# Performance work log

Measured on AMD Instinct MI355X. Metric: run time of the kernel, lower is better.

## Reference

```python
import jax, jax.numpy as jnp
import numpy as np
import math

D = 768      # dim_model
H = 12       # num_heads
DK = D // H  # dim_q = dim_k = 64
F = 3072     # dim_feedforward
B, S = 4, 2048
EPS = 1e-5


def layer_norm(x, gamma, beta):
    mu = jnp.mean(x, axis=-1, keepdims=True)
    var = jnp.mean(jnp.square(x - mu), axis=-1, keepdims=True)
    return (x - mu) * jax.lax.rsqrt(var + EPS) * gamma + beta


def setup_inputs() -> dict:
    key = jax.random.key(0)
    ks = jax.random.split(key, 16)
    s = 0.02
    return {
        "source": jax.random.normal(ks[0], (B, S, D), jnp.float32),
        # per-head QKV projections stacked over heads: [H, D, DK]
        "Wq": jax.random.normal(ks[1], (H, D, DK), jnp.float32) * s,
        "bq": jnp.zeros((H, DK), jnp.float32),
        "Wk": jax.random.normal(ks[2], (H, D, DK), jnp.float32) * s,
        "bk": jnp.zeros((H, DK), jnp.float32),
        "Wv": jax.random.normal(ks[3], (H, D, DK), jnp.float32) * s,
        "bv": jnp.zeros((H, DK), jnp.float32),
        "Wo": jax.random.normal(ks[4], (H * DK, D), jnp.float32) * s,
        "bo": jnp.zeros((D,), jnp.float32),
        "g1": jnp.ones((D,), jnp.float32),
        "be1": jnp.zeros((D,), jnp.float32),
        "W1": jax.random.normal(ks[5], (D, F), jnp.float32) * s,
        "bf1": jnp.zeros((F,), jnp.float32),
        "W2": jax.random.normal(ks[6], (F, D), jnp.float32) * s,
        "bf2": jnp.zeros((D,), jnp.float32),
        "g2": jnp.ones((D,), jnp.float32),
        "be2": jnp.zeros((D,), jnp.float32),
    }


def reference(source, Wq, bq, Wk, bk, Wv, bv, Wo, bo, g1, be1, W1, bf1, W2, bf2, g2, be2):
    x = source
    # batched-over-heads QKV (original loops over heads; same math)
    q = jnp.einsum("bsd,hdk->bhsk", x, Wq) + bq[:, None, :]
    k = jnp.einsum("bsd,hdk->bhsk", x, Wk) + bk[:, None, :]
    v = jnp.einsum("bsd,hdk->bhsk", x, Wv) + bv[:, None, :]
    scale = math.sqrt(DK)
    scores = jnp.einsum("bhsk,bhtk->bhst", q, k) / scale  # [B,H,S,S]
    probs = jax.nn.softmax(scores, axis=-1)
    attn = jnp.einsum("bhst,bhtk->bhsk", probs, v)        # [B,H,S,DK]
    # concat heads along feature dim: [B,S,H*DK]
    cat = attn.transpose(0, 2, 1, 3).reshape(B, S, H * DK)
    mha = cat @ Wo + bo
    x1 = layer_norm(x + mha, g1, be1)  # dropout=0 / eval mode
    ffn = jax.nn.relu(x1 @ W1 + bf1) @ W2 + bf2
    return layer_norm(x1 + ffn, g2, be2)
```

## Files before the change

### kernel.cpp

```cpp
#include <hip/hip_runtime.h>
#include <stdint.h>

#define B_ 4
#define S_ 2048
#define D_ 768
#define H_ 12
#define DK_ 64
#define F_ 3072

typedef __bf16 bf16x8 __attribute__((ext_vector_type(8)));
typedef unsigned short u16x8 __attribute__((ext_vector_type(8)));
typedef float f32x4 __attribute__((ext_vector_type(4)));

__device__ inline unsigned short f2bf(float f) {
    union { float f; unsigned u; } v; v.f = f;
    unsigned r = (v.u + 0x7FFFu + ((v.u >> 16) & 1u)) >> 16;
    return (unsigned short)r;
}
__device__ inline float b2f(unsigned short u) {
    union { unsigned u; float f; } v; v.u = ((unsigned)u) << 16;
    return v.f;
}
__device__ inline bf16x8 as_bf(u16x8 v) { return __builtin_bit_cast(bf16x8, v); }
__device__ inline f32x4 mfma16(u16x8 a, u16x8 b, f32x4 c) {
    return __builtin_amdgcn_mfma_f32_16x16x32_bf16(as_bf(a), as_bf(b), c, 0, 0, 0);
}
__device__ inline void gld16(const unsigned short* g, unsigned short* l) {
    __builtin_amdgcn_global_load_lds(
        (__attribute__((address_space(1))) void*)(unsigned short*)g,
        (__attribute__((address_space(3))) void*)l, 16, 0, 0);
}
__device__ inline float fast_exp2(float x) { return __builtin_amdgcn_exp2f(x); }

__global__ __launch_bounds__(256) void prep_k(const float* __restrict__ src,
                                              unsigned short* __restrict__ XBF,
                                              const float* __restrict__ bq,
                                              const float* __restrict__ bk,
                                              const float* __restrict__ bv,
                                              float* __restrict__ BQKV,
                                              const float* __restrict__ Wq,
                                              const float* __restrict__ Wk,
                                              const float* __restrict__ Wv,
                                              const float* __restrict__ Wo,
                                              const float* __restrict__ W1,
                                              const float* __restrict__ W2,
                                              unsigned short* __restrict__ WQT,
                                              unsigned short* __restrict__ WOT,
                                              unsigned short* __restrict__ W1T,
                                              unsigned short* __restrict__ W2T) {
    __shared__ float tile[32][33];
    int bid = blockIdx.x;
    const int t = threadIdx.x;

    if (bid < 6144) {
        int i = (bid * 256 + t) * 4;
        float4 v = *(const float4*)(src + i);
        XBF[i] = f2bf(v.x); XBF[i+1] = f2bf(v.y); XBF[i+2] = f2bf(v.z); XBF[i+3] = f2bf(v.w);
        return;
    }
    bid -= 6144;
    if (bid < 9) {
        int i = bid * 256 + t;
        if (i < 2304) {
            const float* s = (i < 768) ? bq : (i < 1536 ? bk : bv);
            BQKV[i] = s[i % 768];
        }
        return;
    }
    bid -= 9;

    const float* ip; unsigned short* op;
    int inRS, outRS, bx, by;
    if (bid < 1728) {
        int sel = bid / 576; int rem = bid - sel * 576;
        int z = rem / 48; int r2 = rem - z * 48;
        by = r2 >> 1; bx = r2 & 1;
        ip  = (sel == 0 ? Wq : (sel == 1 ? Wk : Wv)) + (long)z * 49152;
        op  = WQT + (long)sel * 589824 + (long)z * 49152;
        inRS = 64; outRS = 768;
    } else {
        bid -= 1728;
        if (bid < 576) {
            by = bid / 24; bx = bid - by * 24;
            ip = Wo; op = WOT; inRS = 768; outRS = 768;
        } else {
            bid -= 576;
            if (bid < 2304) {
                by = bid / 96; bx = bid - by * 96;
                ip = W1; op = W1T; inRS = 3072; outRS = 768;
            } else {
                bid -= 2304;
                by = bid / 24; bx = bid - by * 24;
                ip = W2; op = W2T; inRS = 768; outRS = 3072;
            }
        }
    }
    const int c0 = bx * 32, r0 = by * 32;
    const int tx = t & 31, ty = t >> 5;
    #pragma unroll
    for (int i = 0; i < 32; i += 8)
        tile[ty + i][tx] = ip[(long)(r0 + ty + i) * inRS + c0 + tx];
    __syncthreads();
    #pragma unroll
    for (int i = 0; i < 32; i += 8)
        op[(long)(c0 + ty + i) * outRS + r0 + tx] = f2bf(tile[tx][ty + i]);
}

template<bool OUTBF, bool RELU, bool HASRES, bool SPLIT2>
__global__ __launch_bounds__(256, 3) void gemm_k(const unsigned short* __restrict__ A,
                                                 const unsigned short* __restrict__ Bt,
                                                 const float* __restrict__ bias,
                                                 const float* __restrict__ res,
                                                 void* __restrict__ outp,
                                                 float* __restrict__ outp2,
                                                 int M, int N, int K) {
    __shared__ unsigned short As[8192];
    __shared__ unsigned short Bs[8192];
    const int tid = threadIdx.x;
    const int w = tid >> 6, lane = tid & 63;
    const int m = lane & 15, quad = lane >> 4;
    const int wm = (w >> 1) * 64, wn = (w & 1) * 64;
    const long m0 = (long)blockIdx.x * 128, n0 = (long)blockIdx.y * 128;

    int koff = 0, kend = K;
    bool lead = true;
    if (SPLIT2) {
        const int Kh = K >> 1, z = blockIdx.z;
        koff = z * Kh; kend = koff + Kh; lead = (z == 0);
    }

    const int rowc = tid >> 2, colc = (tid & 3) * 8;
    const unsigned short* aG0 = A + (m0 + rowc) * K + colc;
    const unsigned short* aG1 = A + (m0 + rowc + 64) * K + colc;
    const unsigned short* bG0 = Bt + (n0 + rowc) * K + colc;
    const unsigned short* bG1 = Bt + (n0 + rowc + 64) * K + colc;

    const f32x4 fz = {0.f, 0.f, 0.f, 0.f};
    f32x4 acc[4][4];
    #pragma unroll
    for (int i = 0; i < 4; i++)
        #pragma unroll
        for (int j = 0; j < 4; j++) acc[i][j] = fz;

    for (int k0 = koff; k0 < kend; k0 += 64) {
        __syncthreads();
        #pragma unroll
        for (int ks = 0; ks < 2; ks++) {
            const int kc = k0 + ks * 32;
            gld16(aG0 + kc, As + ks*4096 + w*512);
            gld16(aG1 + kc, As + ks*4096 + 2048 + w*512);
            gld16(bG0 + kc, Bs + ks*4096 + w*512);
            gld16(bG1 + kc, Bs + ks*4096 + 2048 + w*512);
        }
        __syncthreads();
        #pragma unroll
        for (int ks = 0; ks < 2; ks++) {
            u16x8 af[4], bfr[4];
            #pragma unroll
            for (int i = 0; i < 4; i++) af[i] = *(const u16x8*)&As[ks*4096 + (wm + i*16 + m)*32 + quad*8];
            #pragma unroll
            for (int j = 0; j < 4; j++) bfr[j] = *(const u16x8*)&Bs[ks*4096 + (wn + j*16 + m)*32 + quad*8];
            #pragma unroll
            for (int i = 0; i < 4; i++)
                #pragma unroll
                for (int j = 0; j < 4; j++)
                    acc[i][j] = mfma16(af[i], bfr[j], acc[i][j]);
        }
    }

    #pragma unroll
    for (int j = 0; j < 4; j++) {
        const long col = n0 + wn + j*16 + m;
        const float bv = lead ? bias[col] : 0.0f;
        #pragma unroll
        for (int i = 0; i < 4; i++) {
            #pragma unroll
            for (int r = 0; r < 4; r++) {
                const long row = m0 + wm + i*16 + quad*4 + r;
                float v = acc[i][j][r] + bv;
                if (HASRES) { if (lead) v += res[row * N + col]; }
                if (RELU)   v = fmaxf(v, 0.0f);
                if (SPLIT2) {
                    float* o = lead ? (float*)outp : outp2;
                    o[row * N + col] = v;
                } else if (OUTBF) {
                    ((unsigned short*)outp)[row * N + col] = f2bf(v);
                } else {
                    ((float*)outp)[row * N + col] = v;
                }
            }
        }
    }
}

__global__ __launch_bounds__(256, 3) void attn_k(const unsigned short* __restrict__ qkv,
                                                 unsigned short* __restrict__ cat) {
    __shared__ unsigned short Kl[2][4096];
    __shared__ unsigned short Vt[2][64 * 68];
    __shared__ unsigned short Pl[4][32 * 72];

    const int tid = threadIdx.x, w = tid >> 6, lane = tid & 63;
    const int m = lane & 15, quad = lane >> 4;
    const int b = blockIdx.y / H_, h = blockIdx.y % H_;
    const int q0 = blockIdx.x * 128 + w * 32;
    const long rb = (long)b * S_;
    const int LD = 3 * D_;

    const unsigned short* kb = qkv + rb * (long)LD + h * DK_ + D_;
    const unsigned short* vb = qkv + rb * (long)LD + h * DK_ + 2 * D_;

    const int krow = tid >> 2, kcol = (tid & 3) * 8;

    const float QS = 0.125f * 1.4426950408889634f;
    u16x8 qf[2][2];
    #pragma unroll
    for (int s = 0; s < 2; s++)
        #pragma unroll
        for (int ks = 0; ks < 2; ks++) {
            const unsigned short* qp = qkv + (rb + q0 + s*16 + m) * (long)LD + h*DK_ + ks*32 + quad*8;
            u16x8 raw = *(const u16x8*)qp;
            u16x8 sc;
            #pragma unroll
            for (int j = 0; j < 8; j++) sc[j] = f2bf(b2f(raw[j]) * QS);
            qf[s][ks] = sc;
        }

    const int vpr = (tid >> 3) * 2;
    const int vd  = (tid & 7) * 8;

    gld16(kb + (long)krow * LD + kcol,      &Kl[0][w * 512]);
    gld16(kb + (long)krow * LD + 32 + kcol, &Kl[0][2048 + w * 512]);
    {
        u16x8 v0 = *(const u16x8*)(vb + (long)(vpr)     * LD + vd);
        u16x8 v1 = *(const u16x8*)(vb + (long)(vpr + 1) * LD + vd);
        #pragma unroll
        for (int j = 0; j < 8; j++) {
            unsigned pk = (unsigned)v0[j] | ((unsigned)v1[j] << 16);
            *(unsigned*)&Vt[0][(vd + j)*68 + vpr] = pk;
        }
    }

    const f32x4 fz = {0.f, 0.f, 0.f, 0.f};
    float lrow[2] = {0.f, 0.f};
    f32x4 oacc[2][4];
    #pragma unroll
    for (int s = 0; s < 2; s++)
        #pragma unroll
        for (int o = 0; o < 4; o++) oacc[s][o] = fz;

    const int NC = S_ / 64;
    for (int c = 0; c < NC; c++) {
        const int kv0 = c * 64;
        const bool havenext = (c + 1 < NC);
        __syncthreads();

        const unsigned short* kcur = Kl[c & 1];
        const unsigned short* vcur = Vt[c & 1];

        if (havenext) {
            unsigned short* kn_ = Kl[(c + 1) & 1];
            gld16(kb + (long)(kv0 + 64 + krow) * LD + kcol,      kn_ + w * 512);
            gld16(kb + (long)(kv0 + 64 + krow) * LD + 32 + kcol, kn_ + 2048 + w * 512);
        }
        const int kvn = havenext ? kv0 + 64 : kv0;
        u16x8 nv0 = *(const u16x8*)(vb + (long)(kvn + vpr)     * LD + vd);
        u16x8 nv1 = *(const u16x8*)(vb + (long)(kvn + vpr + 1) * LD + vd);

        f32x4 st[2][4];
        #pragma unroll
        for (int s = 0; s < 2; s++)
            #pragma unroll
            for (int t = 0; t < 4; t++) st[s][t] = fz;
        #pragma unroll
        for (int t = 0; t < 4; t++) {
            u16x8 kf0 = *(const u16x8*)&kcur[(t*16 + m)*32 + quad*8];
            u16x8 kf1 = *(const u16x8*)&kcur[2048 + (t*16 + m)*32 + quad*8];
            st[0][t] = mfma16(kf0, qf[0][0], st[0][t]);
            st[0][t] = mfma16(kf1, qf[0][1], st[0][t]);
            st[1][t] = mfma16(kf0, qf[1][0], st[1][t]);
            st[1][t] = mfma16(kf1, qf[1][1], st[1][t]);
        }

        #pragma unroll
        for (int s = 0; s < 2; s++) {
            float su = 0.f;
            #pragma unroll
            for (int t = 0; t < 4; t++) {
                float p0 = fast_exp2(st[s][t][0]);
                float p1 = fast_exp2(st[s][t][1]);
                float p2 = fast_exp2(st[s][t][2]);
                float p3 = fast_exp2(st[s][t][3]);
                su += (p0 + p1) + (p2 + p3);
                unsigned a0 = __builtin_bit_cast(unsigned, p0) + 0x8000u;
                unsigned a1 = __builtin_bit_cast(unsigned, p1) + 0x8000u;
                unsigned a2 = __builtin_bit_cast(unsigned, p2) + 0x8000u;
                unsigned a3 = __builtin_bit_cast(unsigned, p3) + 0x8000u;
                uint2 pk;
                pk.x = __builtin_amdgcn_perm(a1, a0, 0x07060302u);
                pk.y = __builtin_amdgcn_perm(a3, a2, 0x07060302u);
                *(uint2*)&Pl[w][(s*16 + m)*72 + t*16 + quad*4] = pk;
            }
            lrow[s] += su;
        }

        __asm__ volatile("s_waitcnt lgkmcnt(0)" ::: "memory");

        u16x8 pf[2][2];
        #pragma unroll
        for (int s = 0; s < 2; s++)
            #pragma unroll
            for (int ks = 0; ks < 2; ks++)
                pf[s][ks] = *(const u16x8*)&Pl[w][(s*16 + m)*72 + ks*32 + quad*8];

        #pragma unroll
        for (int o = 0; o < 4; o++)
            #pragma unroll
            for (int ks = 0; ks < 2; ks++) {
                union { u16x8 v; uint2 d[2]; } vf;
                vf.d[0] = *(const uint2*)&vcur[(o*16 + m)*68 + ks*32 + quad*8];
                vf.d[1] = *(const uint2*)&vcur[(o*16 + m)*68 + ks*32 + quad*8 + 4];
                oacc[0][o] = mfma16(vf.v, pf[0][ks], oacc[0][o]);
                oacc[1][o] = mfma16(vf.v, pf[1][ks], oacc[1][o]);
            }

        if (havenext) {
            unsigned short* vtn = Vt[(c + 1) & 1];
            #pragma unroll
            for (int j = 0; j < 8; j++) {
                unsigned pk = (unsigned)nv0[j] | ((unsigned)nv1[j] << 16);
                *(unsigned*)&vtn[(vd + j)*68 + vpr] = pk;
            }
        }
    }

    #pragma unroll
    for (int s = 0; s < 2; s++) {
        lrow[s] += __shfl_xor(lrow[s], 16);
        lrow[s] += __shfl_xor(lrow[s], 32);
        const float inv = 1.0f / lrow[s];
        unsigned short* cp = cat + (rb + q0 + s*16 + m) * (long)D_ + h*DK_ + quad*4;
        #pragma unroll
        for (int o = 0; o < 4; o++) {
            unsigned short h0 = f2bf(oacc[s][o][0] * inv);
            unsigned short h1 = f2bf(oacc[s][o][1] * inv);
            unsigned short h2 = f2bf(oacc[s][o][2] * inv);
            unsigned short h3 = f2bf(oacc[s][o][3] * inv);
            uint2 pk;
            pk.x = (unsigned)h0 | ((unsigned)h1 << 16);
            pk.y = (unsigned)h2 | ((unsigned)h3 << 16);
            *(uint2*)(cp + o*16) = pk;
        }
    }
}

__global__ __launch_bounds__(256) void ln_k(const float* __restrict__ in,
                                            const float* __restrict__ in2,
                                            const float* __restrict__ g,
                                            const float* __restrict__ be,
                                            float* __restrict__ outF,
                                            unsigned short* __restrict__ outB) {
    __shared__ float sm[4], sm2[4];
    const int t = threadIdx.x, w = t >> 6, lane = t & 63;
    const long row = blockIdx.x;
    const float* x = in + row * D_;
    float v0 = x[t], v1 = x[t + 256], v2 = x[t + 512];
    if (in2) {
        const float* y = in2 + row * D_;
        v0 += y[t]; v1 += y[t + 256]; v2 += y[t + 512];
    }
    float s = v0 + v1 + v2;
    float s2 = v0*v0 + v1*v1 + v2*v2;
    #pragma unroll
    for (int off = 32; off >= 1; off >>= 1) {
        s  += __shfl_xor(s,  off, 64);
        s2 += __shfl_xor(s2, off, 64);
    }
    if (lane == 0) { sm[w] = s; sm2[w] = s2; }
    __syncthreads();
    s  = sm[0] + sm[1] + sm[2] + sm[3];
    s2 = sm2[0] + sm2[1] + sm2[2] + sm2[3];
    const float mu = s * (1.0f / D_);
    float var = s2 * (1.0f / D_) - mu * mu;
    var = fmaxf(var, 0.0f);
    const float rs = rsqrtf(var + 1e-5f);
    #pragma unroll
    for (int i = 0; i < 3; i++) {
        const int idx = t + i * 256;
        const float vv = (i == 0 ? v0 : (i == 1 ? v1 : v2));
        const float y = (vv - mu) * rs * g[idx] + be[idx];
        if (outF) outF[row * D_ + idx] = y;
        if (outB) outB[row * D_ + idx] = f2bf(y);
    }
}

extern "C" void kernel_launch(void* const* d_in, const int* in_sizes, int n_in,
                              void* d_out, int out_size, void* d_ws, size_t ws_size,
                              hipStream_t stream) {
    const float* src = (const float*)d_in[0];
    const float* Wq  = (const float*)d_in[1];
    const float* bq  = (const float*)d_in[2];
    const float* Wk  = (const float*)d_in[3];
    const float* bk  = (const float*)d_in[4];
    const float* Wv  = (const float*)d_in[5];
    const float* bv  = (const float*)d_in[6];
    const float* Wo  = (const float*)d_in[7];
    const float* bo  = (const float*)d_in[8];
    const float* g1  = (const float*)d_in[9];
    const float* be1 = (const float*)d_in[10];
    const float* W1  = (const float*)d_in[11];
    const float* bf1 = (const float*)d_in[12];
    const float* W2  = (const float*)d_in[13];
    const float* bf2 = (const float*)d_in[14];
    const float* g2  = (const float*)d_in[15];
    const float* be2 = (const float*)d_in[16];
    float* out = (float*)d_out;

    char* ws = (char*)d_ws;
    unsigned short* XBF  = (unsigned short*)(ws);
    float*          P1F2 = (float*)(ws);
    unsigned short* CAT  = (unsigned short*)(ws + 12582912);
    unsigned short* QKV  = (unsigned short*)(ws + 25165824);
    float*          Y1   = (float*)(ws + 25165824);
    unsigned short* WQT  = (unsigned short*)(ws + 62914560);
    unsigned short* WOT  = (unsigned short*)(ws + 66453504);
    unsigned short* W1T  = (unsigned short*)(ws + 67633152);
    unsigned short* W2T  = (unsigned short*)(ws + 72351744);
    float*          BQKV = (float*)(ws + 77070336);
    float*          X1R  = (float*)(ws + 77079552);
    unsigned short* X1B  = (unsigned short*)(ws + 102245376);
    unsigned short* Hb   = (unsigned short*)(ws + 114828288);

    prep_k<<<dim3(13065), 256, 0, stream>>>(src, XBF, bq, bk, bv, BQKV,
                                            Wq, Wk, Wv, Wo, W1, W2,
                                            WQT, WOT, W1T, W2T);

    gemm_k<true, false, false, false><<<dim3(64, 18), 256, 0, stream>>>(
        XBF, WQT, BQKV, nullptr, QKV, nullptr, 8192, 2304, 768);
    attn_k<<<dim3(16, 48), 256, 0, stream>>>(QKV, CAT);
    gemm_k<false, false, true, false><<<dim3(64, 6), 256, 0, stream>>>(
        CAT, WOT, bo, src, Y1, nullptr, 8192, 768, 768);
    ln_k<<<dim3(8192), 256, 0, stream>>>(Y1, nullptr, g1, be1, X1R, X1B);
    gemm_k<true, true, false, false><<<dim3(64, 24), 256, 0, stream>>>(
        X1B, W1T, bf1, nullptr, Hb, nullptr, 8192, 3072, 768);
    gemm_k<false, false, true, true><<<dim3(64, 6, 2), 256, 0, stream>>>(
        Hb, W2T, bf2, X1R, Y1, P1F2, 8192, 768, 3072);
    ln_k<<<dim3(8192), 256, 0, stream>>>(Y1, P1F2, g2, be2, out, nullptr);
}
```

Measured before the change: 394.7 us.

## Store split-K partials and residual in bf16, split-K the Wo GEMM

Both split-K GEMM partial outputs and the residual stream between layers are now stored as bf16 instead of fp32. The Wo projection also switches to a 2-way split-K launch, so it gets more blocks, and the first layernorm now sums the two bf16 partials. The aim is to cut memory traffic in the GEMM epilogues and layernorm reads, and to give the Wo GEMM more parallelism. The cost is precision: partial sums and the residual x1 are rounded to bf16 before normalization, and the FFN residual now uses the bf16 X1B.

```diff
diff --git a/kernel.cpp b/kernel.cpp
--- a/kernel.cpp
+++ b/kernel.cpp
@@ -106,13 +106,13 @@
         op[(long)(c0 + ty + i) * outRS + r0 + tx] = f2bf(tile[tx][ty + i]);
 }
 
-template<bool OUTBF, bool RELU, bool HASRES, bool SPLIT2>
+template<bool OUTBF, bool RELU, int RESMODE, bool SPLIT2>
 __global__ __launch_bounds__(256, 3) void gemm_k(const unsigned short* __restrict__ A,
                                                  const unsigned short* __restrict__ Bt,
                                                  const float* __restrict__ bias,
-                                                 const float* __restrict__ res,
+                                                 const void* __restrict__ res,
                                                  void* __restrict__ outp,
-                                                 float* __restrict__ outp2,
+                                                 unsigned short* __restrict__ outp2,
                                                  int M, int N, int K) {
     __shared__ unsigned short As[8192];
     __shared__ unsigned short Bs[8192];
@@ -178,11 +178,12 @@
             for (int r = 0; r < 4; r++) {
                 const long row = m0 + wm + i*16 + quad*4 + r;
                 float v = acc[i][j][r] + bv;
-                if (HASRES) { if (lead) v += res[row * N + col]; }
+                if (RESMODE == 1) { if (lead) v += ((const float*)res)[row * N + col]; }
+                if (RESMODE == 2) { if (lead) v += b2f(((const unsigned short*)res)[row * N + col]); }
                 if (RELU)   v = fmaxf(v, 0.0f);
                 if (SPLIT2) {
-                    float* o = lead ? (float*)outp : outp2;
-                    o[row * N + col] = v;
+                    unsigned short* o = lead ? (unsigned short*)outp : outp2;
+                    o[row * N + col] = f2bf(v);
                 } else if (OUTBF) {
                     ((unsigned short*)outp)[row * N + col] = f2bf(v);
                 } else {
@@ -353,8 +354,8 @@
     }
 }
 
-__global__ __launch_bounds__(256) void ln_k(const float* __restrict__ in,
-                                            const float* __restrict__ in2,
+__global__ __launch_bounds__(256) void ln_k(const unsigned short* __restrict__ in1,
+                                            const unsigned short* __restrict__ in2,
                                             const float* __restrict__ g,
                                             const float* __restrict__ be,
                                             float* __restrict__ outF,
@@ -362,12 +363,15 @@
     __shared__ float sm[4], sm2[4];
     const int t = threadIdx.x, w = t >> 6, lane = t & 63;
     const long row = blockIdx.x;
-    const float* x = in + row * D_;
-    float v0 = x[t], v1 = x[t + 256], v2 = x[t + 512];
-    if (in2) {
-        const float* y = in2 + row * D_;
-        v0 += y[t]; v1 += y[t + 256]; v2 += y[t + 512];
-    }
+    const unsigned short* x = in1 + row * D_;
+    const unsigned short* y = in2 + row * D_;
+    const unsigned a01 = *(const unsigned*)(x + 2*t);
+    const unsigned b01 = *(const unsigned*)(y + 2*t);
+    const unsigned a2  = x[512 + t];
+    const unsigned b2v = y[512 + t];
+    float v0 = b2f((unsigned short)(a01 & 0xffff)) + b2f((unsigned short)(b01 & 0xffff));
+    float v1 = b2f((unsigned short)(a01 >> 16))    + b2f((unsigned short)(b01 >> 16));
+    float v2 = b2f((unsigned short)a2)             + b2f((unsigned short)b2v);
     float s = v0 + v1 + v2;
     float s2 = v0*v0 + v1*v1 + v2*v2;
     #pragma unroll
@@ -383,13 +387,19 @@
     float var = s2 * (1.0f / D_) - mu * mu;
     var = fmaxf(var, 0.0f);
     const float rs = rsqrtf(var + 1e-5f);
-    #pragma unroll
-    for (int i = 0; i < 3; i++) {
-        const int idx = t + i * 256;
-        const float vv = (i == 0 ? v0 : (i == 1 ? v1 : v2));
-        const float y = (vv - mu) * rs * g[idx] + be[idx];
-        if (outF) outF[row * D_ + idx] = y;
-        if (outB) outB[row * D_ + idx] = f2bf(y);
+    const int i0 = 2*t, i1 = 2*t + 1, i2 = 512 + t;
+    const float y0 = (v0 - mu) * rs * g[i0] + be[i0];
+    const float y1 = (v1 - mu) * rs * g[i1] + be[i1];
+    const float y2 = (v2 - mu) * rs * g[i2] + be[i2];
+    if (outF) {
+        float2 p; p.x = y0; p.y = y1;
+        *(float2*)(outF + row * D_ + i0) = p;
+        outF[row * D_ + i2] = y2;
+    }
+    if (outB) {
+        unsigned pk = (unsigned)f2bf(y0) | ((unsigned)f2bf(y1) << 16);
+        *(unsigned*)(outB + row * D_ + i0) = pk;
+        outB[row * D_ + i2] = f2bf(y2);
     }
 }
 
@@ -417,16 +427,17 @@
 
     char* ws = (char*)d_ws;
     unsigned short* XBF  = (unsigned short*)(ws);
-    float*          P1F2 = (float*)(ws);
+    unsigned short* P0b  = (unsigned short*)(ws);
     unsigned short* CAT  = (unsigned short*)(ws + 12582912);
+    unsigned short* P1b  = (unsigned short*)(ws + 12582912);
     unsigned short* QKV  = (unsigned short*)(ws + 25165824);
-    float*          Y1   = (float*)(ws + 25165824);
+    unsigned short* Y0b  = (unsigned short*)(ws + 25165824);
+    unsigned short* Y1b  = (unsigned short*)(ws + 37748736);
     unsigned short* WQT  = (unsigned short*)(ws + 62914560);
     unsigned short* WOT  = (unsigned short*)(ws + 66453504);
     unsigned short* W1T  = (unsigned short*)(ws + 67633152);
     unsigned short* W2T  = (unsigned short*)(ws + 72351744);
     float*          BQKV = (float*)(ws + 77070336);
-    float*          X1R  = (float*)(ws + 77079552);
     unsigned short* X1B  = (unsigned short*)(ws + 102245376);
     unsigned short* Hb   = (unsigned short*)(ws + 114828288);
 
@@ -434,15 +445,15 @@
                                             Wq, Wk, Wv, Wo, W1, W2,
                                             WQT, WOT, W1T, W2T);
 
-    gemm_k<true, false, false, false><<<dim3(64, 18), 256, 0, stream>>>(
+    gemm_k<true, false, 0, false><<<dim3(64, 18), 256, 0, stream>>>(
         XBF, WQT, BQKV, nullptr, QKV, nullptr, 8192, 2304, 768);
     attn_k<<<dim3(16, 48), 256, 0, stream>>>(QKV, CAT);
-    gemm_k<false, false, true, false><<<dim3(64, 6), 256, 0, stream>>>(
-        CAT, WOT, bo, src, Y1, nullptr, 8192, 768, 768);
-    ln_k<<<dim3(8192), 256, 0, stream>>>(Y1, nullptr, g1, be1, X1R, X1B);
-    gemm_k<true, true, false, false><<<dim3(64, 24), 256, 0, stream>>>(
+    gemm_k<true, false, 1, true><<<dim3(64, 6, 2), 256, 0, stream>>>(
+        CAT, WOT, bo, src, Y0b, Y1b, 8192, 768, 768);
+    ln_k<<<dim3(8192), 256, 0, stream>>>(Y0b, Y1b, g1, be1, nullptr, X1B);
+    gemm_k<true, true, 0, false><<<dim3(64, 24), 256, 0, stream>>>(
         X1B, W1T, bf1, nullptr, Hb, nullptr, 8192, 3072, 768);
-    gemm_k<false, false, true, true><<<dim3(64, 6, 2), 256, 0, stream>>>(
-        Hb, W2T, bf2, X1R, Y1, P1F2, 8192, 768, 3072);
-    ln_k<<<dim3(8192), 256, 0, stream>>>(Y1, P1F2, g2, be2, out, nullptr);
-}
+    gemm_k<true, false, 2, true><<<dim3(64, 6, 2), 256, 0, stream>>>(
+        Hb, W2T, bf2, X1B, P0b, P1b, 8192, 768, 3072);
+    ln_k<<<dim3(8192), 256, 0, stream>>>(P0b, P1b, g2, be2, out, nullptr);
+}
```

After: 402.5 us. No clear change (+2.0%).
